# Optimization experiments

Measured on AMD Instinct MI355X. Metric: run time of the kernel, lower is better.

The kernel has to match this reference:

```python
import jax, jax.numpy as jnp
import numpy as np

VOCAB = 8192
NT = 10        # spike encoder n_timesteps
N = 2048       # n_neurons
CA3 = 2048     # hippocampus CA3 size
S = 1024       # seq_len / context_length
SPARSITY = 0.05
LR = 0.01      # learning_rate * association_strength


def setup_inputs() -> dict:
    key = jax.random.key(0)
    k1, k2, k3, k4, k5 = jax.random.split(key, 5)
    token_ids = jax.random.randint(k1, (1, S), 0, VOCAB)                      # [batch=1, seq]
    sdr_table = jax.random.uniform(k2, (VOCAB, NT, N), dtype=jnp.float32)     # SDR encoder table
    pos_enc = jax.random.uniform(k3, (S, NT, N), dtype=jnp.float32)           # oscillatory position spikes (pre-threshold)
    w_hippo = jax.random.normal(k4, (CA3, N), dtype=jnp.float32) / np.sqrt(N).astype(np.float32)
    assoc_w = jax.random.normal(k5, (CA3, CA3), dtype=jnp.float32) * 0.01     # WEIGHT_INIT_SCALE_RECURRENT gaussian
    return {"token_ids": token_ids, "sdr_table": sdr_table, "pos_enc": pos_enc,
            "w_hippo": w_hippo, "assoc_w": assoc_w}


def reference(token_ids, sdr_table, pos_enc, w_hippo, assoc_w):
    """encode_sequence(learn=True): spike-encode each token, modulate by position
    spikes, run hippocampus, and sequentially Hebbian-update association weights.
    Returns final association weight matrix [CA3, CA3]."""
    tok_spikes = (sdr_table[token_ids[0]] < SPARSITY).astype(jnp.float32)
    # Position spikes (as_spikes=True -> binary) -> [S, NT, N]
    pos_spikes = (pos_enc < SPARSITY).astype(jnp.float32)
    # combined_spikes = token * (1 + 0.5 * position); sum over timesteps -> [S, N]
    hippo_input = (tok_spikes * (1.0 + 0.5 * pos_spikes)).sum(axis=1)
    # Hippocampus CA3 spikes: linear projection + threshold -> binary pattern [S, CA3]
    ca3_patterns = (hippo_input @ w_hippo.T > 0.0).astype(jnp.float32)

    # Sequential Hebbian association learning: W += lr * outer(post, pre), row-renorm.
    def step(W, pre_post):
        pre, post = pre_post
        W = W + LR * jnp.outer(post, pre)
        norm = jnp.maximum(jnp.linalg.norm(W, axis=1, keepdims=True), 1.0)
        return W / norm, None

    W_final, _ = jax.lax.scan(step, assoc_w, (ca3_patterns[:-1], ca3_patterns[1:]))
    return W_final
```

## Files before the change

kernel.cpp:

```cpp
#include <hip/hip_runtime.h>
#include <hip/hip_bf16.h>

#define NT    10
#define NN    2048
#define CA3C  2048
#define SEQ   1024
#define SPARS 0.05f
#define LRC   0.01f

typedef float          f32x4  __attribute__((ext_vector_type(4)));
typedef short          bf16x8 __attribute__((ext_vector_type(8)));
typedef unsigned short u16x4  __attribute__((ext_vector_type(4)));
typedef unsigned short u16x8  __attribute__((ext_vector_type(8)));

__device__ __forceinline__ unsigned short f2bf(float f) {
    unsigned u = __float_as_uint(f);
    u += 0x7FFFu + ((u >> 16) & 1u);
    return (unsigned short)(u >> 16);
}
__device__ __forceinline__ float bf2f(unsigned short h) {
    return __uint_as_float(((unsigned)h) << 16);
}

__global__ __launch_bounds__(256) void k_hippo(const int* __restrict__ tok,
        const float* __restrict__ sdr, const float* __restrict__ pos,
        unsigned short* __restrict__ Hh) {
    int s = blockIdx.x;
    int n = (blockIdx.y * 256 + threadIdx.x) * 4;
    const float* sp = sdr + (long)tok[s] * (NT * NN) + n;
    const float* pp = pos + (long)s * (NT * NN) + n;
    float a0 = 0.f, a1 = 0.f, a2 = 0.f, a3 = 0.f;
    #pragma unroll
    for (int t = 0; t < NT; ++t) {
        float4 sv = *(const float4*)(sp + t * NN);
        float4 pv = *(const float4*)(pp + t * NN);
        if (sv.x < SPARS) a0 += (pv.x < SPARS) ? 1.5f : 1.0f;
        if (sv.y < SPARS) a1 += (pv.y < SPARS) ? 1.5f : 1.0f;
        if (sv.z < SPARS) a2 += (pv.z < SPARS) ? 1.5f : 1.0f;
        if (sv.w < SPARS) a3 += (pv.w < SPARS) ? 1.5f : 1.0f;
    }
    u16x4 o = { f2bf(a0), f2bf(a1), f2bf(a2), f2bf(a3) };
    *(u16x4*)(Hh + (long)s * NN + n) = o;
}

__global__ __launch_bounds__(256) void k_split(const float* __restrict__ src,
        unsigned short* __restrict__ hi, unsigned short* __restrict__ lo) {
    long i = ((long)blockIdx.x * 256 + threadIdx.x) * 8;
    f32x4 x0 = *(const f32x4*)(src + i);
    f32x4 x1 = *(const f32x4*)(src + i + 4);
    float xs[8] = {x0.x, x0.y, x0.z, x0.w, x1.x, x1.y, x1.z, x1.w};
    u16x8 h, l;
    #pragma unroll
    for (int j = 0; j < 8; ++j) {
        unsigned short hb = f2bf(xs[j]);
        h[j] = hb;
        l[j] = f2bf(xs[j] - bf2f(hb));
    }
    *(u16x8*)(hi + i) = h;
    if (lo) *(u16x8*)(lo + i) = l;
}

#define SPLIT_NONE 0
#define SPLIT_A    1
#define SPLIT_B    2

template<int MODE>
__global__ __launch_bounds__(256, 1) void k_mgemm(
        const unsigned short* __restrict__ A0, const unsigned short* __restrict__ A1,
        const unsigned short* __restrict__ Bh, const unsigned short* __restrict__ B1,
        float* __restrict__ C, int M, int N, int K,
        const float* __restrict__ Wadd, const float* __restrict__ af) {
    __shared__ unsigned short LA[128 * 70], LB[128 * 70], LX[128 * 70];
    int tid = threadIdx.x, wid = tid >> 6, l = tid & 63;
    int m0 = blockIdx.y * 128, n0 = blockIdx.x * 128;
    int wr = wid >> 1, wc = wid & 1;
    int fr = l & 15, fk = l >> 4;
    f32x4 acc[4][4] = {};
    int srow = wid * 8 + (l >> 3);
    int scol = (l & 7) * 8;
    bf16x8 ra[4], rb[4], rx[4];
    #pragma unroll
    for (int i = 0; i < 4; ++i) {
        int row = i * 32 + srow;
        ra[i] = *(const bf16x8*)(A0 + (long)(m0 + row) * K + scol);
        rb[i] = *(const bf16x8*)(Bh + (long)(n0 + row) * K + scol);
        if (MODE == SPLIT_A) rx[i] = *(const bf16x8*)(A1 + (long)(m0 + row) * K + scol);
        if (MODE == SPLIT_B) rx[i] = *(const bf16x8*)(B1 + (long)(n0 + row) * K + scol);
    }
    for (int k0 = 0; k0 < K; k0 += 64) {
        __syncthreads();
        #pragma unroll
        for (int i = 0; i < 4; ++i) {
            int row = i * 32 + srow;
            *(bf16x8*)&LA[row * 70 + scol] = ra[i];
            *(bf16x8*)&LB[row * 70 + scol] = rb[i];
            if (MODE != SPLIT_NONE) *(bf16x8*)&LX[row * 70 + scol] = rx[i];
        }
        __syncthreads();
        if (k0 + 64 < K) {
            #pragma unroll
            for (int i = 0; i < 4; ++i) {
                int row = i * 32 + srow;
                ra[i] = *(const bf16x8*)(A0 + (long)(m0 + row) * K + k0 + 64 + scol);
                rb[i] = *(const bf16x8*)(Bh + (long)(n0 + row) * K + k0 + 64 + scol);
                if (MODE == SPLIT_A) rx[i] = *(const bf16x8*)(A1 + (long)(m0 + row) * K + k0 + 64 + scol);
                if (MODE == SPLIT_B) rx[i] = *(const bf16x8*)(B1 + (long)(n0 + row) * K + k0 + 64 + scol);
            }
        }
        #pragma unroll
        for (int ks = 0; ks < 2; ++ks) {
            bf16x8 av[4], bv[4], xv[4];
            #pragma unroll
            for (int t = 0; t < 4; ++t) {
                av[t] = *(const bf16x8*)&LA[(wr * 64 + t * 16 + fr) * 70 + ks * 32 + fk * 8];
                bv[t] = *(const bf16x8*)&LB[(wc * 64 + t * 16 + fr) * 70 + ks * 32 + fk * 8];
                if (MODE == SPLIT_A) xv[t] = *(const bf16x8*)&LX[(wr * 64 + t * 16 + fr) * 70 + ks * 32 + fk * 8];
                if (MODE == SPLIT_B) xv[t] = *(const bf16x8*)&LX[(wc * 64 + t * 16 + fr) * 70 + ks * 32 + fk * 8];
            }
            #pragma unroll
            for (int mt = 0; mt < 4; ++mt)
                #pragma unroll
                for (int nt = 0; nt < 4; ++nt) {
                    acc[mt][nt] = __builtin_amdgcn_mfma_f32_16x16x32_bf16(av[mt], bv[nt], acc[mt][nt], 0, 0, 0);
                    if (MODE == SPLIT_A)
                        acc[mt][nt] = __builtin_amdgcn_mfma_f32_16x16x32_bf16(xv[mt], bv[nt], acc[mt][nt], 0, 0, 0);
                    if (MODE == SPLIT_B)
                        acc[mt][nt] = __builtin_amdgcn_mfma_f32_16x16x32_bf16(av[mt], xv[nt], acc[mt][nt], 0, 0, 0);
                }
        }
    }
    int drb = (l >> 4) * 4;
    #pragma unroll
    for (int mt = 0; mt < 4; ++mt)
        #pragma unroll
        for (int nt = 0; nt < 4; ++nt)
            #pragma unroll
            for (int e = 0; e < 4; ++e) {
                int row = m0 + wr * 64 + mt * 16 + drb + e;
                int cc  = n0 + wc * 64 + nt * 16 + (l & 15);
                float v = acc[mt][nt][e];
                if (Wadd) v = fmaf(af[row], Wadd[(long)row * N + cc], v);
                C[(long)row * N + cc] = v;
            }
}

__global__ void k_zero(unsigned* cnt) { if (threadIdx.x == 0) *cnt = 0; }

__global__ __launch_bounds__(256) void k_fixflag(const float* __restrict__ dots,
        unsigned* __restrict__ list, unsigned* __restrict__ cnt) {
    int i = blockIdx.x * 256 + threadIdx.x;
    int lane = threadIdx.x & 63;
    bool f = fabsf(dots[i]) < 1e-3f;
    unsigned long long m = __ballot(f);
    if (m == 0) return;
    unsigned b0 = 0;
    if (lane == 0) b0 = atomicAdd(cnt, (unsigned)__popcll(m));
    b0 = __shfl(b0, 0, 64);
    if (f) {
        unsigned rank = (unsigned)__popcll(m & ((1ull << lane) - 1ull));
        list[b0 + rank] = (unsigned)i;
    }
}

__global__ __launch_bounds__(64) void k_fix64(const unsigned* __restrict__ list,
        const unsigned* __restrict__ cnt, const unsigned short* __restrict__ Hh,
        const float* __restrict__ w, float* __restrict__ dots) {
    int lane = threadIdx.x;
    unsigned n = *cnt;
    for (unsigned idx = blockIdx.x; idx < n; idx += gridDim.x) {
        unsigned i = list[idx];
        int s = (int)(i >> 11), c = (int)(i & 2047);
        const unsigned short* hr = Hh + (long)s * NN;
        const float* wr = w + (long)c * NN;
        double a = 0.0;
        #pragma unroll
        for (int j = 0; j < 8; ++j) {
            int k = j * 256 + lane * 4;
            f32x4 wv = *(const f32x4*)(wr + k);
            u16x4 hv = *(const u16x4*)(hr + k);
            a += (double)bf2f(hv.x) * (double)wv.x + (double)bf2f(hv.y) * (double)wv.y
               + (double)bf2f(hv.z) * (double)wv.z + (double)bf2f(hv.w) * (double)wv.w;
        }
        #pragma unroll
        for (int o = 1; o < 64; o <<= 1) a += __shfl_xor(a, o, 64);
        if (lane == 0) dots[i] = (a > 0.0) ? 1.0f : -1.0f;
    }
}

__global__ __launch_bounds__(64) void k_pack(const float* __restrict__ dots,
        unsigned* __restrict__ preT, float* __restrict__ popf,
        unsigned short* __restrict__ Xb) {
    int s = blockIdx.x;
    int w = threadIdx.x;
    const float* row = dots + (long)s * CA3C + w * 32;
    unsigned short* xrow = Xb + (long)s * CA3C + w * 32;
    unsigned m = 0;
    #pragma unroll
    for (int j4 = 0; j4 < 8; ++j4) {
        f32x4 v = *(const f32x4*)(row + j4 * 4);
        u16x4 xb;
        xb.x = v.x > 0.f ? 0x3F80 : 0; xb.y = v.y > 0.f ? 0x3F80 : 0;
        xb.z = v.z > 0.f ? 0x3F80 : 0; xb.w = v.w > 0.f ? 0x3F80 : 0;
        m |= (v.x > 0.f ? 1u : 0u) << (j4 * 4 + 0);
        m |= (v.y > 0.f ? 1u : 0u) << (j4 * 4 + 1);
        m |= (v.z > 0.f ? 1u : 0u) << (j4 * 4 + 2);
        m |= (v.w > 0.f ? 1u : 0u) << (j4 * 4 + 3);
        *(u16x4*)(xrow + j4 * 4) = xb;
    }
    preT[w * SEQ + s] = m;
    int pc = __popc(m);
    #pragma unroll
    for (int o = 1; o < 64; o <<= 1) pc += __shfl_xor(pc, o, 64);
    if (w == 0) popf[s] = (float)pc;
}

__global__ __launch_bounds__(256) void k_packpost(const float* __restrict__ dots,
        unsigned* __restrict__ postT) {
    __shared__ unsigned long long masks[4][64];
    int wid = threadIdx.x >> 6, lane = threadIdx.x & 63;
    int tile = blockIdx.x * 4 + wid;
    int rg = tile & 31, sg = tile >> 5;
    int r0 = rg * 64;
    #pragma unroll 8
    for (int k = 0; k < 64; ++k) {
        int s = sg * 64 + k;
        float d = (s < SEQ - 1) ? dots[(long)(s + 1) * CA3C + r0 + lane] : -1.f;
        unsigned long long m = __ballot(d > 0.f);
        if (lane == 0) masks[wid][k] = m;
    }
    unsigned w0 = 0, w1 = 0;
    #pragma unroll
    for (int k = 0; k < 32; ++k) {
        w0 |= (unsigned)((masks[wid][k]      >> lane) & 1ull) << k;
        w1 |= (unsigned)((masks[wid][k + 32] >> lane) & 1ull) << k;
    }
    postT[(r0 + lane) * 32 + sg * 2]     = w0;
    postT[(r0 + lane) * 32 + sg * 2 + 1] = w1;
}

__global__ __launch_bounds__(256) void k_transpose(const unsigned short* __restrict__ Xb,
        unsigned short* __restrict__ XbT) {
    __shared__ unsigned short t[64][72];
    int s0 = blockIdx.x * 64, n0 = blockIdx.y * 64;
    int tx = threadIdx.x & 63, ty = threadIdx.x >> 6;
    #pragma unroll
    for (int ii = 0; ii < 16; ++ii) {
        int i = ty + ii * 4;
        t[i][tx] = Xb[(long)(s0 + i) * CA3C + n0 + tx];
    }
    __syncthreads();
    #pragma unroll
    for (int ii = 0; ii < 16; ++ii) {
        int i = ty + ii * 4;
        XbT[(long)(n0 + i) * SEQ + s0 + tx] = t[tx][i];
    }
}

__global__ __launch_bounds__(256) void k_gram(const unsigned* __restrict__ preT,
        float* __restrict__ G, unsigned short* __restrict__ Gbh,
        unsigned short* __restrict__ Gbl) {
    int i = blockIdx.x;
    int t = threadIdx.x;
    int a0 = 0, a1 = 0, a2 = 0, a3 = 0;
    #pragma unroll 8
    for (int w = 0; w < 64; ++w) {
        unsigned ri = preT[w * SEQ + i];
        const unsigned* pr = preT + w * SEQ;
        a0 += __popc(ri & pr[t]);
        a1 += __popc(ri & pr[t + 256]);
        a2 += __popc(ri & pr[t + 512]);
        a3 += __popc(ri & pr[t + 768]);
    }
    long base = (long)i * SEQ;
    int vi[4] = {a0, a1, a2, a3};
    #pragma unroll
    for (int q = 0; q < 4; ++q) {
        long o = base + t + q * 256;
        float v = (float)vi[q];
        unsigned short h = f2bf(v);
        G[o] = v;
        Gbh[o] = h;
        Gbl[o] = f2bf(v - bf2f(h));
    }
}

__device__ __forceinline__ float wave_sum64(float x) {
    #define DPPADD(ctrl, rmask) \
        x += __int_as_float(__builtin_amdgcn_update_dpp(0, __float_as_int(x), ctrl, rmask, 0xF, true))
    DPPADD(0xB1, 0xF);
    DPPADD(0x4E, 0xF);
    DPPADD(0x141, 0xF);
    DPPADD(0x140, 0xF);
    DPPADD(0x142, 0xA);
    DPPADD(0x143, 0xC);
    #undef DPPADD
    return __int_as_float(__builtin_amdgcn_readlane(__float_as_int(x), 63));
}

__global__ __launch_bounds__(256) void k_scan2(const float* __restrict__ W0,
        const float* __restrict__ B0, const float* __restrict__ G,
        const unsigned short* __restrict__ Gbh, const unsigned short* __restrict__ Gbl,
        const unsigned* __restrict__ postT, const float* __restrict__ popf,
        float* __restrict__ coef, float* __restrict__ alphaf) {
    __shared__ float Gd[64][68];
    __shared__ unsigned short BH[4096];
    __shared__ unsigned short BL[4096];
    __shared__ unsigned short CHL[8][1024];
    __shared__ float ctab[4][1024];
    int tid = threadIdx.x, wid = tid >> 6, lane = tid & 63;
    int r = blockIdx.x * 4 + wid;
    int fr = lane & 15, fk = lane >> 4;
    int nl = tid >> 2, seg = tid & 3;
    #pragma unroll
    for (int kk = 0; kk < 16; ++kk) ctab[wid][kk * 64 + lane] = 0.f;
    const float* wr = W0 + (long)r * NN + lane * 32;
    f32x4 q0 = *(const f32x4*)(wr +  0), q1 = *(const f32x4*)(wr +  4);
    f32x4 q2 = *(const f32x4*)(wr +  8), q3 = *(const f32x4*)(wr + 12);
    f32x4 q4 = *(const f32x4*)(wr + 16), q5 = *(const f32x4*)(wr + 20);
    f32x4 q6 = *(const f32x4*)(wr + 24), q7 = *(const f32x4*)(wr + 28);
    f32x4 pp = q0*q0 + q1*q1 + q2*q2 + q3*q3 + q4*q4 + q5*q5 + q6*q6 + q7*q7;
    float nu = wave_sum64((pp.x + pp.y) + (pp.z + pp.w));
    float alpha = 1.f, inv_alpha = 1.f;
    { float t = fmaxf(nu, 1.f); alpha *= rsqrtf(t); inv_alpha *= sqrtf(t); nu = fminf(nu, 1.f); }
    float s0 = 1.f;

    bf16x8 ph0, ph1, pl0, pl1;
    for (int b = 0; b < 16; ++b) {
        __syncthreads();
        {
            const float* gs = G + (long)(b * 64 + nl) * SEQ + b * 64 + seg * 16;
            *(f32x4*)&Gd[nl][seg * 16 +  0] = *(const f32x4*)(gs +  0);
            *(f32x4*)&Gd[nl][seg * 16 +  4] = *(const f32x4*)(gs +  4);
            *(f32x4*)&Gd[nl][seg * 16 +  8] = *(const f32x4*)(gs +  8);
            *(f32x4*)&Gd[nl][seg * 16 + 12] = *(const f32x4*)(gs + 12);
        }
        f32x4 acc0 = {}, acc1 = {}, acc2 = {}, acc3 = {};
        if (b > 0) {
            const unsigned short* gh = Gbh + (long)(b * 64 + nl) * SEQ + seg * 16;
            const unsigned short* gl = Gbl + (long)(b * 64 + nl) * SEQ + seg * 16;
            ph0 = *(const bf16x8*)(gh); ph1 = *(const bf16x8*)(gh + 8);
            pl0 = *(const bf16x8*)(gl); pl1 = *(const bf16x8*)(gl + 8);
        }
        for (int ch = 0; ch < b; ++ch) {
            __syncthreads();
            *(bf16x8*)&BH[((seg * 2 + 0) * 64 + nl) * 8] = ph0;
            *(bf16x8*)&BH[((seg * 2 + 1) * 64 + nl) * 8] = ph1;
            *(bf16x8*)&BL[((seg * 2 + 0) * 64 + nl) * 8] = pl0;
            *(bf16x8*)&BL[((seg * 2 + 1) * 64 + nl) * 8] = pl1;
            __syncthreads();
            if (ch + 1 < b) {
                const unsigned short* gh = Gbh + (long)(b * 64 + nl) * SEQ + (ch + 1) * 64 + seg * 16;
                const unsigned short* gl = Gbl + (long)(b * 64 + nl) * SEQ + (ch + 1) * 64 + seg * 16;
                ph0 = *(const bf16x8*)(gh); ph1 = *(const bf16x8*)(gh + 8);
                pl0 = *(const bf16x8*)(gl); pl1 = *(const bf16x8*)(gl + 8);
            }
            #pragma unroll
            for (int kt = 0; kt < 2; ++kt) {
                bf16x8 af = *(const bf16x8*)&CHL[fr & 7][ch * 64 + kt * 32 + fk * 8];
                #define MTILE(T, ACC) { \
                    bf16x8 bh = *(const bf16x8*)&BH[((kt * 4 + fk) * 64 + T * 16 + fr) * 8]; \
                    bf16x8 bl = *(const bf16x8*)&BL[((kt * 4 + fk) * 64 + T * 16 + fr) * 8]; \
                    ACC = __builtin_amdgcn_mfma_f32_16x16x32_bf16(af, bh, ACC, 0, 0, 0); \
                    ACC = __builtin_amdgcn_mfma_f32_16x16x32_bf16(af, bl, ACC, 0, 0, 0); }
                MTILE(0, acc0) MTILE(1, acc1) MTILE(2, acc2) MTILE(3, acc3)
                #undef MTILE
            }
        }
        __syncthreads();
        float t0 = (wid & 1) ? (acc0.z + acc0.w) : (acc0.x + acc0.y);
        float t1 = (wid & 1) ? (acc1.z + acc1.w) : (acc1.x + acc1.y);
        float t2 = (wid & 1) ? (acc2.z + acc2.w) : (acc2.x + acc2.y);
        float t3 = (wid & 1) ? (acc3.z + acc3.w) : (acc3.x + acc3.y);
        int sa = (((wid >> 1) * 16) + fr) * 4;
        float p0 = __int_as_float(__builtin_amdgcn_ds_bpermute(sa, __float_as_int(t0)));
        float p1 = __int_as_float(__builtin_amdgcn_ds_bpermute(sa, __float_as_int(t1)));
        float p2 = __int_as_float(__builtin_amdgcn_ds_bpermute(sa, __float_as_int(t2)));
        float p3 = __int_as_float(__builtin_amdgcn_ds_bpermute(sa, __float_as_int(t3)));
        float u = (fk == 0) ? p0 : (fk == 1) ? p1 : (fk == 2) ? p2 : p3;

        float myB0  = B0[(long)r * SEQ + b * 64 + lane];
        float mypop = popf[b * 64 + lane];
        unsigned long long pm;
        {   unsigned lo = postT[r * 32 + 2 * b], hi = postT[r * 32 + 2 * b + 1];
            pm = ((unsigned long long)(unsigned)__builtin_amdgcn_readfirstlane((int)hi) << 32)
               |  (unsigned long long)(unsigned)__builtin_amdgcn_readfirstlane((int)lo);
        }
        float dacc = fmaf(s0, myB0, u);
        float cj = 0.f;
        #pragma unroll
        for (int j = 0; j < 64; ++j) {
            if ((pm >> j) & 1ull) {
                float dot = __int_as_float(__builtin_amdgcn_readlane(__float_as_int(dacc), j));
                float pj  = __int_as_float(__builtin_amdgcn_readlane(__float_as_int(mypop), j));
                float c = LRC * inv_alpha;
                nu = fmaf(2.f * LRC, alpha * dot, fmaf(LRC * LRC, pj, nu));
                float t = fmaxf(nu, 1.f);
                alpha *= rsqrtf(t); inv_alpha *= sqrtf(t); nu = fminf(nu, 1.f);
                dacc = fmaf(c, Gd[j][lane], dacc);
                cj = (lane == j) ? c : cj;
            }
        }
        ctab[wid][b * 64 + lane] = cj;
        {   unsigned short hh = f2bf(cj);
            CHL[wid * 2 + 0][b * 64 + lane] = hh;
            CHL[wid * 2 + 1][b * 64 + lane] = f2bf(cj - bf2f(hh));
        }
        if (inv_alpha > 1e10f) {
            #pragma unroll 1
            for (int kk = 0; kk <= b; ++kk) {
                float v = ctab[wid][kk * 64 + lane] * alpha;
                ctab[wid][kk * 64 + lane] = v;
                unsigned short hh = f2bf(v);
                CHL[wid * 2 + 0][kk * 64 + lane] = hh;
                CHL[wid * 2 + 1][kk * 64 + lane] = f2bf(v - bf2f(hh));
            }
            s0 *= alpha; alpha = 1.f; inv_alpha = 1.f;
        }
    }
    if (lane == 0) alphaf[r] = alpha * s0;
    #pragma unroll
    for (int kk = 0; kk < 16; ++kk)
        coef[(long)r * SEQ + kk * 64 + lane] = alpha * ctab[wid][kk * 64 + lane];
}

extern "C" void kernel_launch(void* const* d_in, const int* in_sizes, int n_in,
                              void* d_out, int out_size, void* d_ws, size_t ws_size,
                              hipStream_t stream) {
    const int*   tok     = (const int*)d_in[0];
    const float* sdr     = (const float*)d_in[1];
    const float* pos     = (const float*)d_in[2];
    const float* w_hippo = (const float*)d_in[3];
    const float* assoc   = (const float*)d_in[4];
    float* out = (float*)d_out;

    char* ws = (char*)d_ws;
    unsigned short* Hh  = (unsigned short*)(ws);
    float*          G   = (float*)(ws);
    unsigned short* Wh  = (unsigned short*)(ws + (4l << 20));
    unsigned short* Sh  = Wh;
    unsigned short* Ch  = Wh;
    unsigned short* Cl  = (unsigned short*)(ws + (8l << 20));
    unsigned short* Wl  = (unsigned short*)(ws + (12l << 20));
    float*          coef= (float*)(ws + (12l << 20));
    float*          dots= (float*)(ws + (20l << 20));
    float*          B0f = dots;
    unsigned short* Xb  = (unsigned short*)(ws + (28l << 20));
    unsigned short* Gbh = Xb;
    unsigned short* Gbl = (unsigned short*)(ws + (30l << 20));
    unsigned short* XbT = (unsigned short*)(ws + (32l << 20));
    unsigned* preT   = (unsigned*)(ws + (36l << 20));
    unsigned* postT  = (unsigned*)(ws + (36l << 20) + 262144);
    float*    popf   = (float*)(ws + (36l << 20) + 524288);
    float*    alphaf = (float*)(ws + (36l << 20) + 532480);
    unsigned* cnt    = (unsigned*)(ws + (37l << 20));
    unsigned* list   = (unsigned*)(ws + (37l << 20) + 4096);

    k_hippo            <<<dim3(SEQ, 2),   256, 0, stream>>>(tok, sdr, pos, Hh);
    k_split            <<<2048,           256, 0, stream>>>(w_hippo, Wh, Wl);
    k_mgemm<SPLIT_B>   <<<dim3(16, 8),    256, 0, stream>>>(Hh, nullptr, Wh, Wl, dots,
                                                            1024, 2048, 2048, nullptr, nullptr);
    k_zero             <<<1,               64, 0, stream>>>(cnt);
    k_fixflag          <<<8192,           256, 0, stream>>>(dots, list, cnt);
    k_fix64            <<<2048,            64, 0, stream>>>(list, cnt, Hh, w_hippo, dots);
    k_pack             <<<SEQ,             64, 0, stream>>>(dots, preT, popf, Xb);
    k_packpost         <<<128,            256, 0, stream>>>(dots, postT);
    k_transpose        <<<dim3(16, 32),   256, 0, stream>>>(Xb, XbT);
    k_split            <<<2048,           256, 0, stream>>>(assoc, Sh, nullptr);
    k_mgemm<SPLIT_NONE><<<dim3(8, 16),    256, 0, stream>>>(Sh, nullptr, Xb, nullptr, B0f,
                                                            2048, 1024, 2048, nullptr, nullptr);
    k_gram             <<<SEQ,            256, 0, stream>>>(preT, G, Gbh, Gbl);
    k_scan2            <<<512,            256, 0, stream>>>(assoc, B0f, G, Gbh, Gbl,
                                                            postT, popf, coef, alphaf);
    k_split            <<<1024,           256, 0, stream>>>(coef, Ch, Cl);
    k_mgemm<SPLIT_A>   <<<dim3(16, 16),   256, 0, stream>>>(Ch, Cl, XbT, nullptr, out,
                                                            2048, 2048, 1024, assoc, alphaf);
}
```

Baseline: 503.3 us.

## Fuse small kernels, narrow GEMM tiles, double-buffer scan LDS, emit split coefs directly

Folds the counter zeroing into k_hippo, merges the two split launches and the two pack kernels, and has k_scan2 write bf16 hi/lo coefficients directly instead of fp32 coef plus a separate split pass. The GEMM gains a BN template so the first two GEMMs use 64-wide N tiles, doubling block count for better CU occupancy. k_scan2 double-buffers its BH/BL LDS tiles to drop one barrier per chunk, and replaces the fp32 ctab with reconstruction from the bf16 hi/lo pair. That reconstruction may lose a little precision on renormalisation, and extra workspace regions are used.

```diff
diff --git a/kernel.cpp b/kernel.cpp
--- a/kernel.cpp
+++ b/kernel.cpp
@@ -24,7 +24,8 @@
 
 __global__ __launch_bounds__(256) void k_hippo(const int* __restrict__ tok,
         const float* __restrict__ sdr, const float* __restrict__ pos,
-        unsigned short* __restrict__ Hh) {
+        unsigned short* __restrict__ Hh, unsigned* __restrict__ cnt) {
+    if (blockIdx.x == 0 && blockIdx.y == 0 && threadIdx.x == 0) *cnt = 0;
     int s = blockIdx.x;
     int n = (blockIdx.y * 256 + threadIdx.x) * 4;
     const float* sp = sdr + (long)tok[s] * (NT * NN) + n;
@@ -43,9 +44,9 @@
     *(u16x4*)(Hh + (long)s * NN + n) = o;
 }
 
-__global__ __launch_bounds__(256) void k_split(const float* __restrict__ src,
-        unsigned short* __restrict__ hi, unsigned short* __restrict__ lo) {
-    long i = ((long)blockIdx.x * 256 + threadIdx.x) * 8;
+__device__ __forceinline__ void split8(const float* __restrict__ src,
+        unsigned short* __restrict__ hi, unsigned short* __restrict__ lo, long blk) {
+    long i = (blk * 256 + threadIdx.x) * 8;
     f32x4 x0 = *(const f32x4*)(src + i);
     f32x4 x1 = *(const f32x4*)(src + i + 4);
     float xs[8] = {x0.x, x0.y, x0.z, x0.w, x1.x, x1.y, x1.z, x1.w};
@@ -60,67 +61,100 @@
     if (lo) *(u16x8*)(lo + i) = l;
 }
 
+__global__ __launch_bounds__(256) void k_splits(const float* __restrict__ w_hippo,
+        unsigned short* __restrict__ Wh, unsigned short* __restrict__ Wl,
+        const float* __restrict__ assoc, unsigned short* __restrict__ Sh) {
+    long b = blockIdx.x;
+    if (b < 2048) split8(w_hippo, Wh, Wl, b);
+    else         split8(assoc, Sh, nullptr, b - 2048);
+}
+
 #define SPLIT_NONE 0
 #define SPLIT_A    1
 #define SPLIT_B    2
 
-template<int MODE>
+template<int MODE, int BN>
 __global__ __launch_bounds__(256, 1) void k_mgemm(
         const unsigned short* __restrict__ A0, const unsigned short* __restrict__ A1,
         const unsigned short* __restrict__ Bh, const unsigned short* __restrict__ B1,
         float* __restrict__ C, int M, int N, int K,
         const float* __restrict__ Wadd, const float* __restrict__ af) {
-    __shared__ unsigned short LA[128 * 70], LB[128 * 70], LX[128 * 70];
+    constexpr int NTW = BN / 32;
+    constexpr int XR  = (MODE == SPLIT_A) ? 128 : BN;
+    __shared__ unsigned short LA[128 * 70];
+    __shared__ unsigned short LB[BN * 70];
+    __shared__ unsigned short LX[(MODE == SPLIT_NONE) ? 70 : XR * 70];
     int tid = threadIdx.x, wid = tid >> 6, l = tid & 63;
-    int m0 = blockIdx.y * 128, n0 = blockIdx.x * 128;
+    int m0 = blockIdx.y * 128, n0 = blockIdx.x * BN;
     int wr = wid >> 1, wc = wid & 1;
     int fr = l & 15, fk = l >> 4;
-    f32x4 acc[4][4] = {};
+    f32x4 acc[4][NTW] = {};
     int srow = wid * 8 + (l >> 3);
     int scol = (l & 7) * 8;
-    bf16x8 ra[4], rb[4], rx[4];
-    #pragma unroll
-    for (int i = 0; i < 4; ++i) {
-        int row = i * 32 + srow;
-        ra[i] = *(const bf16x8*)(A0 + (long)(m0 + row) * K + scol);
-        rb[i] = *(const bf16x8*)(Bh + (long)(n0 + row) * K + scol);
-        if (MODE == SPLIT_A) rx[i] = *(const bf16x8*)(A1 + (long)(m0 + row) * K + scol);
-        if (MODE == SPLIT_B) rx[i] = *(const bf16x8*)(B1 + (long)(n0 + row) * K + scol);
-    }
+    bf16x8 ra[4], rb[BN / 32], rx[XR / 32];
+    #pragma unroll
+    for (int i = 0; i < 4; ++i)
+        ra[i] = *(const bf16x8*)(A0 + (long)(m0 + i * 32 + srow) * K + scol);
+    #pragma unroll
+    for (int i = 0; i < BN / 32; ++i)
+        rb[i] = *(const bf16x8*)(Bh + (long)(n0 + i * 32 + srow) * K + scol);
+    if (MODE == SPLIT_A)
+        #pragma unroll
+        for (int i = 0; i < XR / 32; ++i)
+            rx[i] = *(const bf16x8*)(A1 + (long)(m0 + i * 32 + srow) * K + scol);
+    if (MODE == SPLIT_B)
+        #pragma unroll
+        for (int i = 0; i < XR / 32; ++i)
+            rx[i] = *(const bf16x8*)(B1 + (long)(n0 + i * 32 + srow) * K + scol);
+
     for (int k0 = 0; k0 < K; k0 += 64) {
         __syncthreads();
         #pragma unroll
-        for (int i = 0; i < 4; ++i) {
-            int row = i * 32 + srow;
-            *(bf16x8*)&LA[row * 70 + scol] = ra[i];
-            *(bf16x8*)&LB[row * 70 + scol] = rb[i];
-            if (MODE != SPLIT_NONE) *(bf16x8*)&LX[row * 70 + scol] = rx[i];
-        }
+        for (int i = 0; i < 4; ++i) *(bf16x8*)&LA[(i * 32 + srow) * 70 + scol] = ra[i];
+        #pragma unroll
+        for (int i = 0; i < BN / 32; ++i) *(bf16x8*)&LB[(i * 32 + srow) * 70 + scol] = rb[i];
+        if (MODE != SPLIT_NONE)
+            #pragma unroll
+            for (int i = 0; i < XR / 32; ++i) *(bf16x8*)&LX[(i * 32 + srow) * 70 + scol] = rx[i];
         __syncthreads();
         if (k0 + 64 < K) {
-            #pragma unroll
-            for (int i = 0; i < 4; ++i) {
-                int row = i * 32 + srow;
-                ra[i] = *(const bf16x8*)(A0 + (long)(m0 + row) * K + k0 + 64 + scol);
-                rb[i] = *(const bf16x8*)(Bh + (long)(n0 + row) * K + k0 + 64 + scol);
-                if (MODE == SPLIT_A) rx[i] = *(const bf16x8*)(A1 + (long)(m0 + row) * K + k0 + 64 + scol);
-                if (MODE == SPLIT_B) rx[i] = *(const bf16x8*)(B1 + (long)(n0 + row) * K + k0 + 64 + scol);
-            }
+            int kn = k0 + 64;
+            #pragma unroll
+            for (int i = 0; i < 4; ++i)
+                ra[i] = *(const bf16x8*)(A0 + (long)(m0 + i * 32 + srow) * K + kn + scol);
+            #pragma unroll
+            for (int i = 0; i < BN / 32; ++i)
+                rb[i] = *(const bf16x8*)(Bh + (long)(n0 + i * 32 + srow) * K + kn + scol);
+            if (MODE == SPLIT_A)
+                #pragma unroll
+                for (int i = 0; i < XR / 32; ++i)
+                    rx[i] = *(const bf16x8*)(A1 + (long)(m0 + i * 32 + srow) * K + kn + scol);
+            if (MODE == SPLIT_B)
+                #pragma unroll
+                for (int i = 0; i < XR / 32; ++i)
+                    rx[i] = *(const bf16x8*)(B1 + (long)(n0 + i * 32 + srow) * K + kn + scol);
         }
         #pragma unroll
         for (int ks = 0; ks < 2; ++ks) {
-            bf16x8 av[4], bv[4], xv[4];
-            #pragma unroll
-            for (int t = 0; t < 4; ++t) {
+            bf16x8 av[4], bv[NTW], xv[4];
+            #pragma unroll
+            for (int t = 0; t < 4; ++t)
                 av[t] = *(const bf16x8*)&LA[(wr * 64 + t * 16 + fr) * 70 + ks * 32 + fk * 8];
-                bv[t] = *(const bf16x8*)&LB[(wc * 64 + t * 16 + fr) * 70 + ks * 32 + fk * 8];
-                if (MODE == SPLIT_A) xv[t] = *(const bf16x8*)&LX[(wr * 64 + t * 16 + fr) * 70 + ks * 32 + fk * 8];
-                if (MODE == SPLIT_B) xv[t] = *(const bf16x8*)&LX[(wc * 64 + t * 16 + fr) * 70 + ks * 32 + fk * 8];
-            }
+            #pragma unroll
+            for (int t = 0; t < NTW; ++t)
+                bv[t] = *(const bf16x8*)&LB[(wc * (BN / 2) + t * 16 + fr) * 70 + ks * 32 + fk * 8];
+            if (MODE == SPLIT_A)
+                #pragma unroll
+                for (int t = 0; t < 4; ++t)
+                    xv[t] = *(const bf16x8*)&LX[(wr * 64 + t * 16 + fr) * 70 + ks * 32 + fk * 8];
+            if (MODE == SPLIT_B)
+                #pragma unroll
+                for (int t = 0; t < NTW; ++t)
+                    xv[t] = *(const bf16x8*)&LX[(wc * (BN / 2) + t * 16 + fr) * 70 + ks * 32 + fk * 8];
             #pragma unroll
             for (int mt = 0; mt < 4; ++mt)
                 #pragma unroll
-                for (int nt = 0; nt < 4; ++nt) {
+                for (int nt = 0; nt < NTW; ++nt) {
                     acc[mt][nt] = __builtin_amdgcn_mfma_f32_16x16x32_bf16(av[mt], bv[nt], acc[mt][nt], 0, 0, 0);
                     if (MODE == SPLIT_A)
                         acc[mt][nt] = __builtin_amdgcn_mfma_f32_16x16x32_bf16(xv[mt], bv[nt], acc[mt][nt], 0, 0, 0);
@@ -133,18 +167,16 @@
     #pragma unroll
     for (int mt = 0; mt < 4; ++mt)
         #pragma unroll
-        for (int nt = 0; nt < 4; ++nt)
+        for (int nt = 0; nt < NTW; ++nt)
             #pragma unroll
             for (int e = 0; e < 4; ++e) {
                 int row = m0 + wr * 64 + mt * 16 + drb + e;
-                int cc  = n0 + wc * 64 + nt * 16 + (l & 15);
+                int cc  = n0 + wc * (BN / 2) + nt * 16 + (l & 15);
                 float v = acc[mt][nt][e];
                 if (Wadd) v = fmaf(af[row], Wadd[(long)row * N + cc], v);
                 C[(long)row * N + cc] = v;
             }
 }
-
-__global__ void k_zero(unsigned* cnt) { if (threadIdx.x == 0) *cnt = 0; }
 
 __global__ __launch_bounds__(256) void k_fixflag(const float* __restrict__ dots,
         unsigned* __restrict__ list, unsigned* __restrict__ cnt) {
@@ -187,55 +219,53 @@
     }
 }
 
-__global__ __launch_bounds__(64) void k_pack(const float* __restrict__ dots,
+__global__ __launch_bounds__(256) void k_packx(const float* __restrict__ dots,
         unsigned* __restrict__ preT, float* __restrict__ popf,
-        unsigned short* __restrict__ Xb) {
-    int s = blockIdx.x;
-    int w = threadIdx.x;
-    const float* row = dots + (long)s * CA3C + w * 32;
-    unsigned short* xrow = Xb + (long)s * CA3C + w * 32;
-    unsigned m = 0;
-    #pragma unroll
-    for (int j4 = 0; j4 < 8; ++j4) {
-        f32x4 v = *(const f32x4*)(row + j4 * 4);
-        u16x4 xb;
-        xb.x = v.x > 0.f ? 0x3F80 : 0; xb.y = v.y > 0.f ? 0x3F80 : 0;
-        xb.z = v.z > 0.f ? 0x3F80 : 0; xb.w = v.w > 0.f ? 0x3F80 : 0;
-        m |= (v.x > 0.f ? 1u : 0u) << (j4 * 4 + 0);
-        m |= (v.y > 0.f ? 1u : 0u) << (j4 * 4 + 1);
-        m |= (v.z > 0.f ? 1u : 0u) << (j4 * 4 + 2);
-        m |= (v.w > 0.f ? 1u : 0u) << (j4 * 4 + 3);
-        *(u16x4*)(xrow + j4 * 4) = xb;
-    }
-    preT[w * SEQ + s] = m;
-    int pc = __popc(m);
-    #pragma unroll
-    for (int o = 1; o < 64; o <<= 1) pc += __shfl_xor(pc, o, 64);
-    if (w == 0) popf[s] = (float)pc;
-}
-
-__global__ __launch_bounds__(256) void k_packpost(const float* __restrict__ dots,
-        unsigned* __restrict__ postT) {
-    __shared__ unsigned long long masks[4][64];
+        unsigned short* __restrict__ Xb, unsigned* __restrict__ postT) {
     int wid = threadIdx.x >> 6, lane = threadIdx.x & 63;
-    int tile = blockIdx.x * 4 + wid;
-    int rg = tile & 31, sg = tile >> 5;
-    int r0 = rg * 64;
-    #pragma unroll 8
-    for (int k = 0; k < 64; ++k) {
-        int s = sg * 64 + k;
-        float d = (s < SEQ - 1) ? dots[(long)(s + 1) * CA3C + r0 + lane] : -1.f;
-        unsigned long long m = __ballot(d > 0.f);
-        if (lane == 0) masks[wid][k] = m;
-    }
-    unsigned w0 = 0, w1 = 0;
-    #pragma unroll
-    for (int k = 0; k < 32; ++k) {
-        w0 |= (unsigned)((masks[wid][k]      >> lane) & 1ull) << k;
-        w1 |= (unsigned)((masks[wid][k + 32] >> lane) & 1ull) << k;
-    }
-    postT[(r0 + lane) * 32 + sg * 2]     = w0;
-    postT[(r0 + lane) * 32 + sg * 2 + 1] = w1;
+    if (blockIdx.x < 256) {
+        int s = blockIdx.x * 4 + wid;
+        const float* row = dots + (long)s * CA3C + lane * 32;
+        unsigned short* xrow = Xb + (long)s * CA3C + lane * 32;
+        unsigned m = 0;
+        #pragma unroll
+        for (int j4 = 0; j4 < 8; ++j4) {
+            f32x4 v = *(const f32x4*)(row + j4 * 4);
+            u16x4 xb;
+            xb.x = v.x > 0.f ? 0x3F80 : 0; xb.y = v.y > 0.f ? 0x3F80 : 0;
+            xb.z = v.z > 0.f ? 0x3F80 : 0; xb.w = v.w > 0.f ? 0x3F80 : 0;
+            m |= (v.x > 0.f ? 1u : 0u) << (j4 * 4 + 0);
+            m |= (v.y > 0.f ? 1u : 0u) << (j4 * 4 + 1);
+            m |= (v.z > 0.f ? 1u : 0u) << (j4 * 4 + 2);
+            m |= (v.w > 0.f ? 1u : 0u) << (j4 * 4 + 3);
+            *(u16x4*)(xrow + j4 * 4) = xb;
+        }
+        preT[lane * SEQ + s] = m;
+        int pc = __popc(m);
+        #pragma unroll
+        for (int o = 1; o < 64; o <<= 1) pc += __shfl_xor(pc, o, 64);
+        if (lane == 0) popf[s] = (float)pc;
+    } else {
+        __shared__ unsigned long long masks[4][64];
+        int tile = (blockIdx.x - 256) * 4 + wid;
+        int rg = tile & 31, sg = tile >> 5;
+        int r0 = rg * 64;
+        #pragma unroll 8
+        for (int k = 0; k < 64; ++k) {
+            int s = sg * 64 + k;
+            float d = (s < SEQ - 1) ? dots[(long)(s + 1) * CA3C + r0 + lane] : -1.f;
+            unsigned long long m = __ballot(d > 0.f);
+            if (lane == 0) masks[wid][k] = m;
+        }
+        unsigned w0 = 0, w1 = 0;
+        #pragma unroll
+        for (int k = 0; k < 32; ++k) {
+            w0 |= (unsigned)((masks[wid][k]      >> lane) & 1ull) << k;
+            w1 |= (unsigned)((masks[wid][k + 32] >> lane) & 1ull) << k;
+        }
+        postT[(r0 + lane) * 32 + sg * 2]     = w0;
+        postT[(r0 + lane) * 32 + sg * 2 + 1] = w1;
+    }
 }
 
 __global__ __launch_bounds__(256) void k_transpose(const unsigned short* __restrict__ Xb,
@@ -301,18 +331,16 @@
         const float* __restrict__ B0, const float* __restrict__ G,
         const unsigned short* __restrict__ Gbh, const unsigned short* __restrict__ Gbl,
         const unsigned* __restrict__ postT, const float* __restrict__ popf,
-        float* __restrict__ coef, float* __restrict__ alphaf) {
+        unsigned short* __restrict__ Ch, unsigned short* __restrict__ Cl,
+        float* __restrict__ alphaf) {
     __shared__ float Gd[64][68];
-    __shared__ unsigned short BH[4096];
-    __shared__ unsigned short BL[4096];
+    __shared__ unsigned short BH[2][4096];
+    __shared__ unsigned short BL[2][4096];
     __shared__ unsigned short CHL[8][1024];
-    __shared__ float ctab[4][1024];
     int tid = threadIdx.x, wid = tid >> 6, lane = tid & 63;
     int r = blockIdx.x * 4 + wid;
     int fr = lane & 15, fk = lane >> 4;
     int nl = tid >> 2, seg = tid & 3;
-    #pragma unroll
-    for (int kk = 0; kk < 16; ++kk) ctab[wid][kk * 64 + lane] = 0.f;
     const float* wr = W0 + (long)r * NN + lane * 32;
     f32x4 q0 = *(const f32x4*)(wr +  0), q1 = *(const f32x4*)(wr +  4);
     f32x4 q2 = *(const f32x4*)(wr +  8), q3 = *(const f32x4*)(wr + 12);
@@ -334,39 +362,47 @@
             *(f32x4*)&Gd[nl][seg * 16 +  8] = *(const f32x4*)(gs +  8);
             *(f32x4*)&Gd[nl][seg * 16 + 12] = *(const f32x4*)(gs + 12);
         }
-        f32x4 acc0 = {}, acc1 = {}, acc2 = {}, acc3 = {};
         if (b > 0) {
             const unsigned short* gh = Gbh + (long)(b * 64 + nl) * SEQ + seg * 16;
             const unsigned short* gl = Gbl + (long)(b * 64 + nl) * SEQ + seg * 16;
             ph0 = *(const bf16x8*)(gh); ph1 = *(const bf16x8*)(gh + 8);
             pl0 = *(const bf16x8*)(gl); pl1 = *(const bf16x8*)(gl + 8);
-        }
+            *(bf16x8*)&BH[0][((seg * 2 + 0) * 64 + nl) * 8] = ph0;
+            *(bf16x8*)&BH[0][((seg * 2 + 1) * 64 + nl) * 8] = ph1;
+            *(bf16x8*)&BL[0][((seg * 2 + 0) * 64 + nl) * 8] = pl0;
+            *(bf16x8*)&BL[0][((seg * 2 + 1) * 64 + nl) * 8] = pl1;
+        }
+        __syncthreads();
+        f32x4 acc0 = {}, acc1 = {}, acc2 = {}, acc3 = {};
         for (int ch = 0; ch < b; ++ch) {
-            __syncthreads();
-            *(bf16x8*)&BH[((seg * 2 + 0) * 64 + nl) * 8] = ph0;
-            *(bf16x8*)&BH[((seg * 2 + 1) * 64 + nl) * 8] = ph1;
-            *(bf16x8*)&BL[((seg * 2 + 0) * 64 + nl) * 8] = pl0;
-            *(bf16x8*)&BL[((seg * 2 + 1) * 64 + nl) * 8] = pl1;
-            __syncthreads();
             if (ch + 1 < b) {
                 const unsigned short* gh = Gbh + (long)(b * 64 + nl) * SEQ + (ch + 1) * 64 + seg * 16;
                 const unsigned short* gl = Gbl + (long)(b * 64 + nl) * SEQ + (ch + 1) * 64 + seg * 16;
                 ph0 = *(const bf16x8*)(gh); ph1 = *(const bf16x8*)(gh + 8);
                 pl0 = *(const bf16x8*)(gl); pl1 = *(const bf16x8*)(gl + 8);
             }
+            const unsigned short* bh = BH[ch & 1];
+            const unsigned short* bl = BL[ch & 1];
             #pragma unroll
             for (int kt = 0; kt < 2; ++kt) {
                 bf16x8 af = *(const bf16x8*)&CHL[fr & 7][ch * 64 + kt * 32 + fk * 8];
                 #define MTILE(T, ACC) { \
-                    bf16x8 bh = *(const bf16x8*)&BH[((kt * 4 + fk) * 64 + T * 16 + fr) * 8]; \
-                    bf16x8 bl = *(const bf16x8*)&BL[((kt * 4 + fk) * 64 + T * 16 + fr) * 8]; \
-                    ACC = __builtin_amdgcn_mfma_f32_16x16x32_bf16(af, bh, ACC, 0, 0, 0); \
-                    ACC = __builtin_amdgcn_mfma_f32_16x16x32_bf16(af, bl, ACC, 0, 0, 0); }
+                    bf16x8 vh = *(const bf16x8*)&bh[((kt * 4 + fk) * 64 + T * 16 + fr) * 8]; \
+                    bf16x8 vl = *(const bf16x8*)&bl[((kt * 4 + fk) * 64 + T * 16 + fr) * 8]; \
+                    ACC = __builtin_amdgcn_mfma_f32_16x16x32_bf16(af, vh, ACC, 0, 0, 0); \
+                    ACC = __builtin_amdgcn_mfma_f32_16x16x32_bf16(af, vl, ACC, 0, 0, 0); }
                 MTILE(0, acc0) MTILE(1, acc1) MTILE(2, acc2) MTILE(3, acc3)
                 #undef MTILE
             }
-        }
-        __syncthreads();
+            if (ch + 1 < b) {
+                int nb = (ch + 1) & 1;
+                *(bf16x8*)&BH[nb][((seg * 2 + 0) * 64 + nl) * 8] = ph0;
+                *(bf16x8*)&BH[nb][((seg * 2 + 1) * 64 + nl) * 8] = ph1;
+                *(bf16x8*)&BL[nb][((seg * 2 + 0) * 64 + nl) * 8] = pl0;
+                *(bf16x8*)&BL[nb][((seg * 2 + 1) * 64 + nl) * 8] = pl1;
+            }
+            __syncthreads();
+        }
         float t0 = (wid & 1) ? (acc0.z + acc0.w) : (acc0.x + acc0.y);
         float t1 = (wid & 1) ? (acc1.z + acc1.w) : (acc1.x + acc1.y);
         float t2 = (wid & 1) ? (acc2.z + acc2.w) : (acc2.x + acc2.y);
@@ -400,7 +436,6 @@
                 cj = (lane == j) ? c : cj;
             }
         }
-        ctab[wid][b * 64 + lane] = cj;
         {   unsigned short hh = f2bf(cj);
             CHL[wid * 2 + 0][b * 64 + lane] = hh;
             CHL[wid * 2 + 1][b * 64 + lane] = f2bf(cj - bf2f(hh));
@@ -408,8 +443,8 @@
         if (inv_alpha > 1e10f) {
             #pragma unroll 1
             for (int kk = 0; kk <= b; ++kk) {
-                float v = ctab[wid][kk * 64 + lane] * alpha;
-                ctab[wid][kk * 64 + lane] = v;
+                float v = (bf2f(CHL[wid * 2 + 0][kk * 64 + lane])
+                         + bf2f(CHL[wid * 2 + 1][kk * 64 + lane])) * alpha;
                 unsigned short hh = f2bf(v);
                 CHL[wid * 2 + 0][kk * 64 + lane] = hh;
                 CHL[wid * 2 + 1][kk * 64 + lane] = f2bf(v - bf2f(hh));
@@ -419,8 +454,13 @@
     }
     if (lane == 0) alphaf[r] = alpha * s0;
     #pragma unroll
-    for (int kk = 0; kk < 16; ++kk)
-        coef[(long)r * SEQ + kk * 64 + lane] = alpha * ctab[wid][kk * 64 + lane];
+    for (int kk = 0; kk < 16; ++kk) {
+        float v = (bf2f(CHL[wid * 2 + 0][kk * 64 + lane])
+                 + bf2f(CHL[wid * 2 + 1][kk * 64 + lane])) * alpha;
+        unsigned short hh = f2bf(v);
+        Ch[(long)r * SEQ + kk * 64 + lane] = hh;
+        Cl[(long)r * SEQ + kk * 64 + lane] = f2bf(v - bf2f(hh));
+    }
 }
 
 extern "C" void kernel_launch(void* const* d_in, const int* in_sizes, int n_in,
@@ -437,11 +477,7 @@
     unsigned short* Hh  = (unsigned short*)(ws);
     float*          G   = (float*)(ws);
     unsigned short* Wh  = (unsigned short*)(ws + (4l << 20));
-    unsigned short* Sh  = Wh;
-    unsigned short* Ch  = Wh;
-    unsigned short* Cl  = (unsigned short*)(ws + (8l << 20));
     unsigned short* Wl  = (unsigned short*)(ws + (12l << 20));
-    float*          coef= (float*)(ws + (12l << 20));
     float*          dots= (float*)(ws + (20l << 20));
     float*          B0f = dots;
     unsigned short* Xb  = (unsigned short*)(ws + (28l << 20));
@@ -454,24 +490,23 @@
     float*    alphaf = (float*)(ws + (36l << 20) + 532480);
     unsigned* cnt    = (unsigned*)(ws + (37l << 20));
     unsigned* list   = (unsigned*)(ws + (37l << 20) + 4096);
-
-    k_hippo            <<<dim3(SEQ, 2),   256, 0, stream>>>(tok, sdr, pos, Hh);
-    k_split            <<<2048,           256, 0, stream>>>(w_hippo, Wh, Wl);
-    k_mgemm<SPLIT_B>   <<<dim3(16, 8),    256, 0, stream>>>(Hh, nullptr, Wh, Wl, dots,
-                                                            1024, 2048, 2048, nullptr, nullptr);
-    k_zero             <<<1,               64, 0, stream>>>(cnt);
-    k_fixflag          <<<8192,           256, 0, stream>>>(dots, list, cnt);
-    k_fix64            <<<2048,            64, 0, stream>>>(list, cnt, Hh, w_hippo, dots);
-    k_pack             <<<SEQ,             64, 0, stream>>>(dots, preT, popf, Xb);
-    k_packpost         <<<128,            256, 0, stream>>>(dots, postT);
-    k_transpose        <<<dim3(16, 32),   256, 0, stream>>>(Xb, XbT);
-    k_split            <<<2048,           256, 0, stream>>>(assoc, Sh, nullptr);
-    k_mgemm<SPLIT_NONE><<<dim3(8, 16),    256, 0, stream>>>(Sh, nullptr, Xb, nullptr, B0f,
-                                                            2048, 1024, 2048, nullptr, nullptr);
-    k_gram             <<<SEQ,            256, 0, stream>>>(preT, G, Gbh, Gbl);
-    k_scan2            <<<512,            256, 0, stream>>>(assoc, B0f, G, Gbh, Gbl,
-                                                            postT, popf, coef, alphaf);
-    k_split            <<<1024,           256, 0, stream>>>(coef, Ch, Cl);
-    k_mgemm<SPLIT_A>   <<<dim3(16, 16),   256, 0, stream>>>(Ch, Cl, XbT, nullptr, out,
-                                                            2048, 2048, 1024, assoc, alphaf);
-}
+    unsigned short* Sh  = (unsigned short*)(ws + (40l << 20));
+    unsigned short* Ch  = (unsigned short*)(ws + (48l << 20));
+    unsigned short* Cl  = (unsigned short*)(ws + (52l << 20));
+
+    k_hippo                <<<dim3(SEQ, 2), 256, 0, stream>>>(tok, sdr, pos, Hh, cnt);
+    k_splits               <<<4096,         256, 0, stream>>>(w_hippo, Wh, Wl, assoc, Sh);
+    k_mgemm<SPLIT_B, 64>   <<<dim3(32, 8),  256, 0, stream>>>(Hh, nullptr, Wh, Wl, dots,
+                                                              1024, 2048, 2048, nullptr, nullptr);
+    k_fixflag              <<<8192,         256, 0, stream>>>(dots, list, cnt);
+    k_fix64                <<<2048,          64, 0, stream>>>(list, cnt, Hh, w_hippo, dots);
+    k_packx                <<<384,          256, 0, stream>>>(dots, preT, popf, Xb, postT);
+    k_transpose            <<<dim3(16, 32), 256, 0, stream>>>(Xb, XbT);
+    k_mgemm<SPLIT_NONE, 64><<<dim3(16, 16), 256, 0, stream>>>(Sh, nullptr, Xb, nullptr, B0f,
+                                                              2048, 1024, 2048, nullptr, nullptr);
+    k_gram                 <<<SEQ,          256, 0, stream>>>(preT, G, Gbh, Gbl);
+    k_scan2                <<<512,          256, 0, stream>>>(assoc, B0f, G, Gbh, Gbl,
+                                                              postT, popf, Ch, Cl, alphaf);
+    k_mgemm<SPLIT_A, 128>  <<<dim3(16, 16), 256, 0, stream>>>(Ch, Cl, XbT, nullptr, out,
+                                                              2048, 2048, 1024, assoc, alphaf);
+}
```

Result: faster. 464.9 us (-7.6%).
